# Kernel optimization log

Measured on AMD Instinct MI355X. Metric: run time of the kernel, lower is better.

Reference implementation:

```python
import jax, jax.numpy as jnp
import numpy as np

K = 1.0          # Lorentz curvature param: x_t^2 - |x_s|^2 = K
SQRT_K = 1.0
EPS = 1e-8
HEADS = 12

def add_time(s):
    t = jnp.sqrt(K + jnp.sum(s * s, axis=-1, keepdims=True))
    return jnp.concatenate([t, s], axis=-1)

def lorentz_ln(x, g, b):
    s = x[..., 1:]
    mu = jnp.mean(s, axis=-1, keepdims=True)
    var = jnp.var(s, axis=-1, keepdims=True)
    s = (s - mu) / jnp.sqrt(var + 1e-5) * g + b
    return add_time(s)

def lorentz_fc(x, W, heads=None, act=None):
    # linear on full Lorentz vector -> space part; time recomputed to stay on manifold
    s = x @ W.T
    if act is not None:
        s = act(s)
    if heads is not None:
        bsz, n, dt = s.shape
        s = s.reshape(bsz, n, heads, dt // heads).transpose(0, 2, 1, 3)  # (b,h,n,hd)
    return add_time(s)

def logmap0(x):
    t, s = x[..., :1], x[..., 1:]
    sn = jnp.sqrt(jnp.sum(s * s, axis=-1, keepdims=True))
    dist = SQRT_K * jnp.arccosh(jnp.maximum(t / SQRT_K, 1.0 + 1e-7))
    u = dist * s / jnp.maximum(sn, EPS)
    return jnp.concatenate([jnp.zeros_like(t), u], axis=-1)

def expmap0(u):
    us = u[..., 1:]
    n = jnp.sqrt(jnp.sum(us * us, axis=-1, keepdims=True))
    nc = jnp.maximum(n, EPS)
    t = SQRT_K * jnp.cosh(n / SQRT_K)
    s = SQRT_K * jnp.sinh(n / SQRT_K) * us / nc
    return jnp.concatenate([t, s], axis=-1)

def ste_clip(x, lo, hi):
    # straight-through estimator: clamp in fwd, identity grad
    return x + jax.lax.stop_gradient(jnp.clip(x, lo, hi) - x)

def ste_max_clamp(x, hi):
    return x + jax.lax.stop_gradient(jnp.minimum(x, hi) - x)

def mha_last_layer(x, Wq, Wk, Wv, Wo, alpha_raw, tau_raw, lambda_raw):
    q = lorentz_fc(x, Wq, heads=HEADS)   # (b,h,n,hd+1)
    k = lorentz_fc(x, Wk, heads=HEADS)
    v = lorentz_fc(x, Wv, heads=HEADS)
    q_t, q_s = q[..., :1], q[..., 1:]
    k_t, k_s = k[..., :1], k[..., 1:]
    # Lorentzian inner product -> hyperbolic pairwise distances
    inner_QK = -q_t @ jnp.swapaxes(k_t, -1, -2) + jnp.einsum('bhid,bhjd->bhij', q_s, k_s)
    raw_cosh = jnp.maximum(-inner_QK / K, 1.0)                # (b,h,n,n)
    is_self = raw_cosh < 1.0 + 1e-5
    safe_cosh = jnp.where(is_self, 2.0, raw_cosh)
    dist_QK = SQRT_K * jnp.arccosh(safe_cosh)
    cosh_OQ = jnp.maximum(q_t / SQRT_K, 1.0 + 1e-7)
    cosh_OK = jnp.maximum(k_t / SQRT_K, 1.0 + 1e-7)
    c_tilde = jnp.minimum(SQRT_K * jnp.arccosh(cosh_OQ), 40.0) / SQRT_K  # (b,h,n,1)
    sinh_QK = jnp.sinh(dist_QK / SQRT_K)
    sinh_OQ = jnp.sinh(c_tilde)
    numer = raw_cosh * cosh_OQ - jnp.swapaxes(cosh_OK, -1, -2)
    raw_Z = numer / (sinh_OQ * sinh_QK)
    Z_safe = jnp.where(is_self, 1.0, ste_clip(raw_Z, -1.0, 1.0))
    alpha = jax.nn.softplus(alpha_raw)
    B = alpha * c_tilde / (1.0 + alpha * c_tilde)
    lam = jax.nn.softplus(lambda_raw)
    d_L = ste_max_clamp(dist_QK, 40.0)   # float32 branch of STE_Dist_Clamp
    log_dist_penalty = -lam * jnp.log1p(d_L * d_L)
    m = 0.1
    entail = jax.nn.softplus(B + Z_safe - m) - jax.nn.softplus(jnp.asarray(-m, B.dtype))
    tau = jax.nn.softplus(tau_raw)
    score = jax.nn.softmax(log_dist_penalty - tau * entail, axis=-1)
    # expmap aggregation: tangent-space weighted mean
    v_tan = logmap0(v)
    agg = jnp.einsum('bhij,bhjd->bhid', score, v_tan)
    agg = agg / (jnp.sum(score, axis=-1, keepdims=True) + 1e-8)
    attn = expmap0(agg).transpose(0, 2, 1, 3)   # (b,n,h,hd+1)
    bsz, n, h, _ = attn.shape
    attn_s = attn[..., 1:].reshape(bsz, n, -1)
    attn_t = attn[..., :1].reshape(bsz, n, -1)
    t_new = jnp.sqrt(jnp.sum(attn_t ** 2, axis=-1, keepdims=True) - (h - 1) * K)
    return lorentz_fc(jnp.concatenate([t_new, attn_s], axis=-1), Wo)


def setup_inputs() -> dict:
    key = jax.random.key(0)
    ks = jax.random.split(key, 8)
    b, n, hidden, mlp_hidden = 4, 1024, 769, 3073
    d = hidden - 1
    xs = jax.random.normal(ks[0], (b, n, d), jnp.float32)
    x = add_time(xs)
    def w(k, o, i):
        return jax.random.normal(k, (o, i), jnp.float32) * (i ** -0.5)
    return {
        'x': x,
        'Wq': w(ks[1], d, hidden), 'Wk': w(ks[2], d, hidden), 'Wv': w(ks[3], d, hidden),
        'Wo': w(ks[4], d, hidden),
        'ln1_g': jnp.ones((d,), jnp.float32), 'ln1_b': jnp.zeros((d,), jnp.float32),
        'ln2_g': jnp.ones((d,), jnp.float32), 'ln2_b': jnp.zeros((d,), jnp.float32),
        'Wm1': w(ks[5], mlp_hidden - 1, hidden), 'Wm2': w(ks[6], d, mlp_hidden),
        'alpha_raw': jnp.zeros((1,), jnp.float32),
        'tau_raw': jnp.zeros((1,), jnp.float32),
        'lambda_raw': jnp.zeros((1,), jnp.float32),
    }


def reference(x, Wq, Wk, Wv, Wo, ln1_g, ln1_b, ln2_g, ln2_b, Wm1, Wm2, alpha_raw, tau_raw, lambda_raw):
    out = mha_last_layer(lorentz_ln(x, ln1_g, ln1_b), Wq, Wk, Wv, Wo, alpha_raw, tau_raw, lambda_raw)
    out = out[..., 1:] + x[..., 1:]                 # residual on space part (DropPath=identity in eval)
    h = lorentz_ln(add_time(out), ln2_g, ln2_b)
    h = lorentz_fc(h, Wm1, act=lambda z: jax.nn.gelu(z, approximate=False))
    h = lorentz_fc(h, Wm2)
    out = h[..., 1:] + out
    return add_time(out)
```

## Files before the change

kernel.cpp:

```cpp
#include <hip/hip_runtime.h>
#include <cstdint>
#include <cstddef>

typedef unsigned short u16;
typedef __attribute__((ext_vector_type(8))) __bf16 bf16x8;
typedef __attribute__((ext_vector_type(4))) float f32x4;
typedef __attribute__((ext_vector_type(4))) short s16x4;

#define SEQ 1024
#define MROWS 4096
#define DDIM 768
#define HID 769
#define KP1 832
#define MLPD 3072
#define KP2 3136
#define NHEADS 12
#define LN2F 0.69314718056f
#define LOG2EF 1.44269504089f

static __device__ __forceinline__ u16 f2bf(float f){
  union { float f; uint32_t u; } v; v.f = f;
  return (u16)((v.u + 0x7FFFu + ((v.u >> 16) & 1u)) >> 16);
}

static __device__ __forceinline__ f32x4 mfma16(bf16x8 a, bf16x8 b, f32x4 c){
  return __builtin_amdgcn_mfma_f32_16x16x32_bf16(a, b, c, 0, 0, 0);
}

static __device__ __forceinline__ f32x4 mfma16k(s16x4 a, s16x4 b, f32x4 c){
  return __builtin_amdgcn_mfma_f32_16x16x16bf16_1k(a, b, c, 0, 0, 0);
}

static __device__ __forceinline__ s16x4 pack4(uint32_t lo, uint32_t hi){
  union { uint2 u; s16x4 v; } cv; cv.u.x = lo; cv.u.y = hi; return cv.v;
}

static __device__ __forceinline__ void async_lds16(const u16* g, u16* l){
  u16* gm = const_cast<u16*>(g);
  __builtin_amdgcn_global_load_lds(
      (__attribute__((address_space(1))) void*)gm,
      (__attribute__((address_space(3))) void*)l, 16, 0, 0);
}

static __device__ __forceinline__ float blk_reduce(float v, float* red, int tid){
  #pragma unroll
  for (int off = 1; off < 64; off <<= 1) v += __shfl_xor(v, off, 64);
  __syncthreads();
  if ((tid & 63) == 0) red[tid >> 6] = v;
  __syncthreads();
  return red[0] + red[1] + red[2] + red[3];
}

static __device__ __forceinline__ float gelu_fast(float z){
  float z2 = z * z;
  float t = __builtin_fmaf(z2, 0.044715f, 1.f);
  float w = z * t * (-2.3022078f);
  float e2 = __builtin_amdgcn_exp2f(w);
  return z * __builtin_amdgcn_rcpf(1.f + e2);
}

static __device__ __forceinline__ void conv_seg(const float* W, u16* O, int idx, int K, int Kp){
  int n = idx / Kp, k = idx - n * Kp;
  O[idx] = (k < K) ? f2bf(W[(size_t)n * K + k]) : (u16)0;
}
__global__ __launch_bounds__(256) void conv_all(const float* __restrict__ Wq, const float* __restrict__ Wk,
    const float* __restrict__ Wv, const float* __restrict__ Wo,
    const float* __restrict__ Wm1, const float* __restrict__ Wm2, u16* __restrict__ dst){
  int b = blockIdx.x, tid = threadIdx.x;
  if (b < 2496){        conv_seg(Wq,  dst,            b*256+tid,         769, 832); }
  else if (b < 4992){   conv_seg(Wk,  dst + 638976,  (b-2496)*256+tid,   769, 832); }
  else if (b < 7488){   conv_seg(Wv,  dst + 1277952, (b-4992)*256+tid,   769, 832); }
  else if (b < 9984){   conv_seg(Wo,  dst + 1916928, (b-7488)*256+tid,   769, 832); }
  else if (b < 19968){  conv_seg(Wm1, dst + 2555904, (b-9984)*256+tid,   769, 832); }
  else {                conv_seg(Wm2, dst + 5111808, (b-19968)*256+tid, 3073, 3136); }
}

__global__ __launch_bounds__(256) void ln_kernel(const float* __restrict__ X, int xstr, int xoff,
    const float* __restrict__ g, const float* __restrict__ b, u16* __restrict__ O){
  __shared__ float red[4];
  int m = blockIdx.x, tid = threadIdx.x;
  const float* xr = X + (size_t)m * xstr + xoff;
  float s[3], y[3];
  float s1 = 0.f, s2 = 0.f;
  #pragma unroll
  for (int j = 0; j < 3; j++){ float v = xr[tid + j*256]; s[j] = v; s1 += v; s2 += v*v; }
  s1 = blk_reduce(s1, red, tid);
  s2 = blk_reduce(s2, red, tid);
  float mu = s1 * (1.f/768.f);
  float var = s2 * (1.f/768.f) - mu*mu;
  float rstd = rsqrtf(var + 1e-5f);
  float q = 0.f;
  #pragma unroll
  for (int j = 0; j < 3; j++){ int i = tid + j*256; y[j] = (s[j]-mu)*rstd*g[i] + b[i]; q += y[j]*y[j]; }
  q = blk_reduce(q, red, tid);
  u16* orow = O + (size_t)m * KP1;
  #pragma unroll
  for (int j = 0; j < 3; j++) orow[1 + tid + j*256] = f2bf(y[j]);
  if (tid == 0) orow[0] = f2bf(sqrtf(1.f + q));
  if (tid < 63) orow[769 + tid] = 0;
}

__global__ __launch_bounds__(256) void ln_sum_kernel(const float* __restrict__ P2,
    const float* __restrict__ x, const float* __restrict__ g, const float* __restrict__ b,
    float* __restrict__ out1, u16* __restrict__ O, float* __restrict__ rsq){
  __shared__ float red[4];
  int m = blockIdx.x, tid = threadIdx.x;
  if (tid == 0) rsq[m] = 0.f;
  float s[3], y[3];
  float s1 = 0.f, s2 = 0.f;
  #pragma unroll
  for (int j = 0; j < 3; j++){
    int col = tid + j*256;
    float v = x[(size_t)m * HID + 1 + col];
    #pragma unroll
    for (int z = 0; z < 2; z++) v += P2[(size_t)z*MROWS*DDIM + (size_t)m*DDIM + col];
    out1[(size_t)m*DDIM + col] = v;
    s[j] = v; s1 += v; s2 += v*v;
  }
  s1 = blk_reduce(s1, red, tid);
  s2 = blk_reduce(s2, red, tid);
  float mu = s1 * (1.f/768.f);
  float var = s2 * (1.f/768.f) - mu*mu;
  float rstd = rsqrtf(var + 1e-5f);
  float q = 0.f;
  #pragma unroll
  for (int j = 0; j < 3; j++){ int i = tid + j*256; y[j] = (s[j]-mu)*rstd*g[i] + b[i]; q += y[j]*y[j]; }
  q = blk_reduce(q, red, tid);
  u16* orow = O + (size_t)m * KP1;
  #pragma unroll
  for (int j = 0; j < 3; j++) orow[1 + tid + j*256] = f2bf(y[j]);
  if (tid == 0) orow[0] = f2bf(sqrtf(1.f + q));
  if (tid < 63) orow[769 + tid] = 0;
}

__global__ __launch_bounds__(256) void gemm64(
    const u16* __restrict__ A, const u16* __restrict__ B,
    float* __restrict__ C, u16* __restrict__ Og, float* __restrict__ rsq,
    int N, int Kp, int gelu)
{
  __shared__ u16 As[128*64];
  __shared__ u16 Bs[64*64];
  int tid = threadIdx.x;
  int wave = tid >> 6, lane = tid & 63;
  int lrow = lane & 15, lq = lane >> 4;
  int m0 = blockIdx.y * 128, n0 = blockIdx.x * 64;
  int wm = wave >> 1, wn = wave & 1;
  int chunks = Kp >> 6;
  int nz = gridDim.z, z = blockIdx.z;
  int base = chunks / nz, rem = chunks - base * nz;
  int begin = z * base + (z < rem ? z : rem);
  int count = base + (z < rem ? 1 : 0);
  f32x4 acc[4][2] = {};
  int srow = lane >> 3;
  int scol = (lane & 7) * 8;
  const u16* Abase = A + (size_t)m0 * Kp;
  const u16* Bbase = B + (size_t)n0 * Kp;
  for (int kc = begin; kc < begin + count; kc++){
    int k0 = kc * 64;
    __syncthreads();
    #pragma unroll
    for (int i = 0; i < 4; i++){
      int s = wave*4 + i;
      async_lds16(Abase + (size_t)(s*8 + srow) * Kp + k0 + scol, As + s*512);
    }
    #pragma unroll
    for (int i = 0; i < 2; i++){
      int s = wave*2 + i;
      async_lds16(Bbase + (size_t)(s*8 + srow) * Kp + k0 + scol, Bs + s*512);
    }
    __syncthreads();
    bf16x8 af[4][2], bfr[2][2];
    #pragma unroll
    for (int t = 0; t < 4; t++)
      #pragma unroll
      for (int kk = 0; kk < 2; kk++)
        af[t][kk] = *(const bf16x8*)(As + (wm*64 + t*16 + lrow)*64 + kk*32 + lq*8);
    #pragma unroll
    for (int t = 0; t < 2; t++)
      #pragma unroll
      for (int kk = 0; kk < 2; kk++)
        bfr[t][kk] = *(const bf16x8*)(Bs + (wn*32 + t*16 + lrow)*64 + kk*32 + lq*8);
    #pragma unroll
    for (int kk = 0; kk < 2; kk++)
      #pragma unroll
      for (int mt = 0; mt < 4; mt++)
        #pragma unroll
        for (int nt = 0; nt < 2; nt++)
          acc[mt][nt] = mfma16(af[mt][kk], bfr[nt][kk], acc[mt][nt]);
  }
  if (gelu == 0){
    C += (size_t)z * MROWS * N;
    #pragma unroll
    for (int mt = 0; mt < 4; mt++)
      #pragma unroll
      for (int nt = 0; nt < 2; nt++){
        int col = n0 + wn*32 + nt*16 + lrow;
        #pragma unroll
        for (int r = 0; r < 4; r++){
          int row = m0 + wm*64 + mt*16 + lq*4 + r;
          C[(size_t)row * N + col] = acc[mt][nt][r];
        }
      }
  } else {
    float ssq[4][4];
    #pragma unroll
    for (int mt = 0; mt < 4; mt++)
      #pragma unroll
      for (int r = 0; r < 4; r++) ssq[mt][r] = 0.f;
    #pragma unroll
    for (int mt = 0; mt < 4; mt++)
      #pragma unroll
      for (int nt = 0; nt < 2; nt++){
        int col = n0 + wn*32 + nt*16 + lrow;
        #pragma unroll
        for (int r = 0; r < 4; r++){
          int row = m0 + wm*64 + mt*16 + lq*4 + r;
          float e = gelu_fast(acc[mt][nt][r]);
          ssq[mt][r] += e*e;
          Og[(size_t)row * KP2 + 1 + col] = f2bf(e);
        }
      }
    #pragma unroll
    for (int mt = 0; mt < 4; mt++)
      #pragma unroll
      for (int r = 0; r < 4; r++){
        float v = ssq[mt][r];
        v += __shfl_xor(v, 1, 64);
        v += __shfl_xor(v, 2, 64);
        v += __shfl_xor(v, 4, 64);
        v += __shfl_xor(v, 8, 64);
        if (lrow == 0)
          atomicAdd(rsq + m0 + wm*64 + mt*16 + lq*4 + r, v);
      }
  }
}

__global__ __launch_bounds__(256) void timecol(const float* __restrict__ rsq, u16* __restrict__ O){
  int idx = blockIdx.x * 256 + threadIdx.x;
  int m = idx >> 6, j = idx & 63;
  if (j == 0) O[(size_t)m * KP2] = f2bf(sqrtf(1.f + rsq[m]));
  else        O[(size_t)m * KP2 + 3072 + j] = 0;
}

__global__ __launch_bounds__(256) void pack_qk(const float* __restrict__ raw,
    u16* __restrict__ Qp, u16* __restrict__ Kpk, float* __restrict__ qt, float* __restrict__ kt)
{
  int wave = threadIdx.x >> 6, lane = threadIdx.x & 63;
  int m = blockIdx.x * 4 + wave;
  int h = blockIdx.y;
  int which = blockIdx.z;
  const float* src = raw + (size_t)m * 2304 + which * 768 + h*64 + lane;
  float v = *src;
  float ss = v*v;
  #pragma unroll
  for (int off = 1; off < 64; off <<= 1) ss += __shfl_xor(ss, off, 64);
  int b = m >> 10, n = m & 1023, bh = b * NHEADS + h;
  u16* dst = (which ? Kpk : Qp) + ((size_t)bh * SEQ + n) * 64 + lane;
  *dst = f2bf(v);
  if (lane == 0) (which ? kt : qt)[bh * SEQ + n] = sqrtf(1.f + ss);
}

__global__ __launch_bounds__(256) void pack_v(const float* __restrict__ vraw, u16* __restrict__ Vf){
  __shared__ float part[256];
  __shared__ float scl[64];
  __shared__ float tile[64][65];
  int tid = threadIdx.x;
  int kb = blockIdx.x, bh = blockIdx.y;
  int b = bh / NHEADS, h = bh - b*NHEADS;
  int kl = tid >> 2;
  int d0 = (tid & 3) * 16;
  int m = b * SEQ + kb * 64 + kl;
  float v[16]; float ss = 0.f;
  const float* src = vraw + (size_t)m * 2304 + h*64 + d0;
  #pragma unroll
  for (int i = 0; i < 16; i++){ v[i] = src[i]; ss += v[i]*v[i]; }
  part[tid] = ss;
  __syncthreads();
  if ((tid & 3) == 0){
    float s2 = part[tid] + part[tid+1] + part[tid+2] + part[tid+3];
    float sn = sqrtf(s2);
    float tv = sqrtf(1.f + s2);
    float ctv = fmaxf(tv, 1.f + 1e-7f);
    float dist = __logf(ctv + sqrtf(fmaxf(ctv*ctv - 1.f, 0.f)));
    scl[kl] = dist / fmaxf(sn, 1e-8f);
  }
  __syncthreads();
  float sc = scl[kl];
  #pragma unroll
  for (int i = 0; i < 16; i++) tile[kl][d0 + i] = v[i] * sc;
  __syncthreads();
  #pragma unroll
  for (int i = 0; i < 2; i++){
    int idx = tid + i*256;
    int ctg_l = idx >> 7;
    int ntp = (idx >> 6) & 1;
    int ln  = idx & 63;
    int lr = ln & 15, lqq = ln >> 4;
    int k0 = ctg_l*16 + lqq*4;
    int dlo = ntp*32 + lr;
    u16 tmp[8];
    #pragma unroll
    for (int j = 0; j < 4; j++){
      tmp[j]     = f2bf(tile[k0+j][dlo]);
      tmp[4+j]   = f2bf(tile[k0+j][dlo+16]);
    }
    u16* dst = Vf + ((((size_t)bh*64 + kb*4 + ctg_l)*2 + ntp)*64 + ln)*8;
    *(uint4*)dst = *(const uint4*)tmp;
  }
}

__global__ __launch_bounds__(256) void attn_kernel(
    const u16* __restrict__ Q, const u16* __restrict__ K, const u16* __restrict__ Vf,
    const float* __restrict__ qt, const float* __restrict__ kt,
    float* __restrict__ pAgg, float* __restrict__ pDen,
    const float* __restrict__ a_raw, const float* __restrict__ t_raw, const float* __restrict__ l_raw)
{
  __shared__ float rv[4][64];
  int tid = threadIdx.x;
  int bh = blockIdx.y, ks = blockIdx.z;
  int qbase = blockIdx.x * 64;
  float alpha = __logf(1.f + __expf(a_raw[0]));
  float tau   = __logf(1.f + __expf(t_raw[0]));
  float lam   = __logf(1.f + __expf(l_raw[0]));
  if (tid < 64){
    float qtv = qt[bh * SEQ + qbase + tid];
    float cq = fmaxf(qtv, 1.f + 1e-7f);
    float A = cq + __builtin_amdgcn_sqrtf(fmaxf(cq*cq - 1.f, 0.f));
    float ct = fminf(__builtin_amdgcn_logf(A) * LN2F, 40.f);
    float e = __expf(ct);
    float sh = 0.5f * (e - __builtin_amdgcn_rcpf(e));
    float ac = alpha * ct;
    rv[0][tid] = qtv;
    rv[1][tid] = cq;
    rv[2][tid] = __builtin_amdgcn_rcpf(sh);
    rv[3][tid] = (ac * __builtin_amdgcn_rcpf(1.f + ac) - 0.1f) * LOG2EF;
  }
  __syncthreads();
  int wave = tid >> 6, lane = tid & 63;
  int lrow = lane & 15, lq = lane >> 4;
  int myrow = wave*16 + lrow;
  float qt_l = rv[0][myrow], cq_l = rv[1][myrow], rri_l = rv[2][myrow], Bw_l = rv[3][myrow];
  const float tbase = tau * 0.92967051f;
  const u16* Qb = Q + ((size_t)bh * SEQ + qbase + wave*16 + lrow) * 64 + lq*8;
  bf16x8 bq0 = *(const bf16x8*)Qb;
  bf16x8 bq1 = *(const bf16x8*)(Qb + 32);
  const u16* Kt = K + (size_t)bh * SEQ * 64 + (size_t)(ks*512 + lrow) * 64 + lq*8;
  const u16* Vp = Vf + (size_t)bh * 65536 + (size_t)(ks*32) * 1024 + lane*8;
  const float* ktp = kt + (size_t)bh * SEQ + ks*512 + lq*4;
  s16x4 ones;
  ones[0] = (short)0x3F80; ones[1] = (short)0x3F80; ones[2] = (short)0x3F80; ones[3] = (short)0x3F80;
  f32x4 o[4] = {};
  f32x4 dacc = {};
  for (int jt = 0; jt < 8; jt++){
    bf16x8 vv[8];
    #pragma unroll
    for (int ct = 0; ct < 4; ct++){
      vv[ct*2]   = *(const bf16x8*)(Vp + ct*1024);
      vv[ct*2+1] = *(const bf16x8*)(Vp + ct*1024 + 512);
    }
    float4 kv[4];
    #pragma unroll
    for (int ct = 0; ct < 4; ct++) kv[ct] = *(const float4*)(ktp + ct*16);
    f32x4 s[4];
    #pragma unroll
    for (int ct = 0; ct < 4; ct++){
      bf16x8 a0 = *(const bf16x8*)(Kt + ct*1024);
      bf16x8 a1 = *(const bf16x8*)(Kt + ct*1024 + 32);
      f32x4 z = {0.f, 0.f, 0.f, 0.f};
      z = mfma16(a0, bq0, z);
      z = mfma16(a1, bq1, z);
      s[ct] = z;
    }
    #pragma unroll
    for (int ct = 0; ct < 4; ct++){
      float4 kvv = kv[ct];
      uint32_t pu[4];
      #pragma unroll
      for (int r = 0; r < 4; r++){
        float ktv = (r == 0) ? kvv.x : (r == 1) ? kvv.y : (r == 2) ? kvv.z : kvv.w;
        float c = fmaxf(__builtin_fmaf(qt_l, ktv, -s[ct][r]), 1.f);
        bool self = c < 1.00001f;
        float ce = self ? 2.f : c;
        float cm1 = __builtin_fmaf(ce, ce, -1.f);
        float rs = __builtin_amdgcn_rsqf(cm1);
        float shq = cm1 * rs;
        float d = __builtin_amdgcn_logf(ce + shq) * LN2F;
        float L1 = __builtin_amdgcn_logf(__builtin_fmaf(d, d, 1.f));
        float Z = __builtin_fmaf(ce, cq_l, -ktv) * rri_l * rs;
        Z = fminf(fmaxf(Z, -1.f), 1.f);
        Z = self ? 1.f : Z;
        float w2 = __builtin_fmaf(Z, LOG2EF, Bw_l);
        float ew = __builtin_amdgcn_exp2f(w2);
        float L2 = __builtin_amdgcn_logf(ew + 1.f);
        float logit = __builtin_fmaf(-lam, L1, __builtin_fmaf(-tau, L2, tbase));
        float p = __builtin_amdgcn_exp2f(logit);
        pu[r] = __float_as_uint(p);
      }
      uint32_t lo = __builtin_amdgcn_perm(pu[1], pu[0], 0x07060302u);
      uint32_t hi = __builtin_amdgcn_perm(pu[3], pu[2], 0x07060302u);
      s16x4 pb = pack4(lo, hi);
      union { bf16x8 v8; s16x4 h[2]; } c0, c1;
      c0.v8 = vv[ct*2]; c1.v8 = vv[ct*2+1];
      o[0] = mfma16k(c0.h[0], pb, o[0]);
      o[1] = mfma16k(c0.h[1], pb, o[1]);
      o[2] = mfma16k(c1.h[0], pb, o[2]);
      o[3] = mfma16k(c1.h[1], pb, o[3]);
      dacc = mfma16k(ones, pb, dacc);
    }
    Kt += 4096; Vp += 4096; ktp += 64;
  }
  size_t rowb = (size_t)(ks*48 + bh) * SEQ + qbase + wave*16 + lrow;
  if (lq == 0) pDen[rowb] = dacc[0];
  #pragma unroll
  for (int nt = 0; nt < 4; nt++){
    float4 ov; ov.x = o[nt][0]; ov.y = o[nt][1]; ov.z = o[nt][2]; ov.w = o[nt][3];
    *(float4*)(pAgg + rowb * 64 + nt*16 + lq*4) = ov;
  }
}

__global__ __launch_bounds__(768) void expmap_pack(const float* __restrict__ pAgg,
    const float* __restrict__ pDen, u16* __restrict__ O){
  __shared__ float th2[NHEADS];
  int m = blockIdx.x, tid = threadIdx.x;
  int h = tid >> 6, lane = tid & 63;
  int b = m >> 10, n = m & 1023, bh = b*NHEADS + h;
  size_t i0 = ((size_t)bh * SEQ + n);
  size_t i1 = ((size_t)(48 + bh) * SEQ + n);
  float d = pDen[i0] + pDen[i1];
  float rden = __builtin_amdgcn_rcpf(d * (1.f + 1e-8f));
  float u = (pAgg[i0*64 + lane] + pAgg[i1*64 + lane]) * rden;
  float n2 = u*u;
  #pragma unroll
  for (int off = 1; off < 64; off <<= 1) n2 += __shfl_xor(n2, off, 64);
  float nn = sqrtf(n2);
  float e = __expf(nn);
  float ch = 0.5f * (e + 1.f/e);
  float sh = 0.5f * (e - 1.f/e);
  float sc = sh / fmaxf(nn, 1e-8f);
  u16* orow = O + (size_t)m * KP1;
  orow[1 + h*64 + lane] = f2bf(u * sc);
  if (lane == 0) th2[h] = ch*ch;
  __syncthreads();
  if (tid == 0){
    float ssum = 0.f;
    #pragma unroll
    for (int i = 0; i < NHEADS; i++) ssum += th2[i];
    orow[0] = f2bf(sqrtf(ssum - 11.f));
  }
  if (tid >= 1 && tid < 64) orow[768 + tid] = 0;
}

__global__ __launch_bounds__(256) void final_sum(const float* __restrict__ P4,
    const float* __restrict__ out1, float* __restrict__ out){
  __shared__ float red[4];
  int m = blockIdx.x, tid = threadIdx.x;
  float v[3]; float s2 = 0.f;
  #pragma unroll
  for (int j = 0; j < 3; j++){
    int col = tid + j*256;
    float t = out1[(size_t)m*DDIM + col];
    #pragma unroll
    for (int z = 0; z < 4; z++) t += P4[(size_t)z*MROWS*DDIM + (size_t)m*DDIM + col];
    v[j] = t; s2 += t*t;
  }
  s2 = blk_reduce(s2, red, tid);
  float* orow = out + (size_t)m * HID;
  if (tid == 0) orow[0] = sqrtf(1.f + s2);
  #pragma unroll
  for (int j = 0; j < 3; j++) orow[1 + tid + j*256] = v[j];
}

extern "C" void kernel_launch(void* const* d_in, const int* in_sizes, int n_in,
                              void* d_out, int out_size, void* d_ws, size_t ws_size,
                              hipStream_t stream)
{
  (void)in_sizes; (void)n_in; (void)out_size; (void)ws_size;
  const float* x   = (const float*)d_in[0];
  const float* Wq  = (const float*)d_in[1];
  const float* Wk  = (const float*)d_in[2];
  const float* Wv  = (const float*)d_in[3];
  const float* Wo  = (const float*)d_in[4];
  const float* g1p = (const float*)d_in[5];
  const float* b1p = (const float*)d_in[6];
  const float* g2p = (const float*)d_in[7];
  const float* b2p = (const float*)d_in[8];
  const float* Wm1 = (const float*)d_in[9];
  const float* Wm2 = (const float*)d_in[10];
  const float* ar  = (const float*)d_in[11];
  const float* tr  = (const float*)d_in[12];
  const float* lr  = (const float*)d_in[13];

  char* ws = (char*)d_ws;
  u16*   wqb  = (u16*)(ws + 0);
  u16*   wob  = (u16*)(ws + 3833856);
  u16*   wm1b = (u16*)(ws + 5111808);
  u16*   wm2b = (u16*)(ws + 10223616);
  u16*   xln  = (u16*)(ws + 15040512);
  float* qkv  = (float*)(ws + 21856256);
  u16*   qp   = (u16*)(ws + 59604992);
  u16*   kpk  = (u16*)(ws + 65896448);
  u16*   vf   = (u16*)(ws + 72187904);
  float* rsq  = (float*)(ws + 78479360);
  float* qtb  = (float*)(ws + 78495744);
  float* ktb  = (float*)(ws + 78692352);
  float* pAgg = (float*)(ws + 78888960);
  float* pDen = (float*)(ws + 104054784);
  u16*   woin = (u16*)(ws + 104448000);
  float* woP  = (float*)(ws + 21856256);
  u16*   ln2b = (u16*)(ws + 78888960);
  u16*   g1b  = (u16*)(ws + 21856256);
  float* out2P= (float*)(ws + 47546368);
  float* out1 = (float*)(ws + 97878016);

  conv_all<<<dim3(29376), 256, 0, stream>>>(Wq, Wk, Wv, Wo, Wm1, Wm2, wqb);
  ln_kernel<<<dim3(4096), 256, 0, stream>>>(x, 769, 1, g1p, b1p, xln);
  gemm64<<<dim3(36, 32, 1), 256, 0, stream>>>(xln, wqb, qkv, nullptr, nullptr, 2304, 832, 0);
  pack_qk<<<dim3(1024, 12, 2), 256, 0, stream>>>(qkv, qp, kpk, qtb, ktb);
  pack_v<<<dim3(16, 48), 256, 0, stream>>>(qkv + 1536, vf);
  attn_kernel<<<dim3(16, 48, 2), 256, 0, stream>>>(qp, kpk, vf, qtb, ktb, pAgg, pDen, ar, tr, lr);
  expmap_pack<<<dim3(4096), 768, 0, stream>>>(pAgg, pDen, woin);
  gemm64<<<dim3(12, 32, 2), 256, 0, stream>>>(woin, wob, woP, nullptr, nullptr, 768, 832, 0);
  ln_sum_kernel<<<dim3(4096), 256, 0, stream>>>(woP, x, g2p, b2p, out1, ln2b, rsq);
  gemm64<<<dim3(48, 32, 1), 256, 0, stream>>>(ln2b, wm1b, nullptr, g1b, rsq, 3072, 832, 1);
  timecol<<<dim3(1024), 256, 0, stream>>>(rsq, g1b);
  gemm64<<<dim3(12, 32, 4), 256, 0, stream>>>(g1b, wm2b, out2P, nullptr, nullptr, 768, 3136, 0);
  final_sum<<<dim3(4096), 256, 0, stream>>>(out2P, out1, (float*)d_out);
}
```

Measured before the change: 396.9 us.

## Pre-swizzle weights into MFMA fragment order and drop LDS staging in GEMMs

The weight conversion kernel now writes the bf16 weights in the exact per-lane MFMA fragment order, tiled by 64-column block and 64-wide K chunk. The GEMM then reads B fragments with coalesced direct global loads and A fragments straight from global memory, removing LDS staging and both barriers per K chunk. The cost is that A reuse across the two N-waves now goes through cache instead of shared memory. A-fragment loads are strided per row, so there is a risk of worse latency hiding and more memory traffic.

Result: slower. 516.4 us (+30.1%).

```diff
diff --git a/kernel.cpp b/kernel.cpp
--- a/kernel.cpp
+++ b/kernel.cpp
@@ -35,13 +35,6 @@
   union { uint2 u; s16x4 v; } cv; cv.u.x = lo; cv.u.y = hi; return cv.v;
 }
 
-static __device__ __forceinline__ void async_lds16(const u16* g, u16* l){
-  u16* gm = const_cast<u16*>(g);
-  __builtin_amdgcn_global_load_lds(
-      (__attribute__((address_space(1))) void*)gm,
-      (__attribute__((address_space(3))) void*)l, 16, 0, 0);
-}
-
 static __device__ __forceinline__ float blk_reduce(float v, float* red, int tid){
   #pragma unroll
   for (int off = 1; off < 64; off <<= 1) v += __shfl_xor(v, off, 64);
@@ -59,20 +52,39 @@
   return z * __builtin_amdgcn_rcpf(1.f + e2);
 }
 
-static __device__ __forceinline__ void conv_seg(const float* W, u16* O, int idx, int K, int Kp){
-  int n = idx / Kp, k = idx - n * Kp;
+static __device__ __forceinline__ void conv_frag(const float* W, u16* O, int idx,
+                                                 int K, int C_){
+  int j = idx & 7;
+  int lane = (idx >> 3) & 63;
+  int lq = lane >> 4, lrow = lane & 15;
+  int rest = idx >> 9;
+  int kk = rest & 1, nt = (rest >> 1) & 1, wn = (rest >> 2) & 1;
+  int kc = (rest >> 3) % C_, nblk = (rest >> 3) / C_;
+  int n = nblk*64 + wn*32 + nt*16 + lrow;
+  int k = kc*64 + kk*32 + lq*8 + j;
   O[idx] = (k < K) ? f2bf(W[(size_t)n * K + k]) : (u16)0;
 }
 __global__ __launch_bounds__(256) void conv_all(const float* __restrict__ Wq, const float* __restrict__ Wk,
     const float* __restrict__ Wv, const float* __restrict__ Wo,
     const float* __restrict__ Wm1, const float* __restrict__ Wm2, u16* __restrict__ dst){
   int b = blockIdx.x, tid = threadIdx.x;
-  if (b < 2496){        conv_seg(Wq,  dst,            b*256+tid,         769, 832); }
-  else if (b < 4992){   conv_seg(Wk,  dst + 638976,  (b-2496)*256+tid,   769, 832); }
-  else if (b < 7488){   conv_seg(Wv,  dst + 1277952, (b-4992)*256+tid,   769, 832); }
-  else if (b < 9984){   conv_seg(Wo,  dst + 1916928, (b-7488)*256+tid,   769, 832); }
-  else if (b < 19968){  conv_seg(Wm1, dst + 2555904, (b-9984)*256+tid,   769, 832); }
-  else {                conv_seg(Wm2, dst + 5111808, (b-19968)*256+tid, 3073, 3136); }
+  if (b < 7488){
+    int idx = b*256 + tid;
+    int j = idx & 7;
+    int lane = (idx >> 3) & 63;
+    int lq = lane >> 4, lrow = lane & 15;
+    int rest = idx >> 9;
+    int kk = rest & 1, nt = (rest >> 1) & 1, wn = (rest >> 2) & 1;
+    int kc = (rest >> 3) % 13, nblk = (rest >> 3) / 13;
+    int n = nblk*64 + wn*32 + nt*16 + lrow;
+    int k = kc*64 + kk*32 + lq*8 + j;
+    const float* W = (n < 768) ? Wq : (n < 1536 ? Wk : Wv);
+    int nn = (n < 768) ? n : (n < 1536 ? n - 768 : n - 1536);
+    dst[idx] = (k < 769) ? f2bf(W[(size_t)nn * 769 + k]) : (u16)0;
+  }
+  else if (b < 9984){  conv_frag(Wo,  dst + 1916928, (b-7488)*256+tid,  769, 13); }
+  else if (b < 19968){ conv_frag(Wm1, dst + 2555904, (b-9984)*256+tid,  769, 13); }
+  else {               conv_frag(Wm2, dst + 5111808, (b-19968)*256+tid, 3073, 49); }
 }
 
 __global__ __launch_bounds__(256) void ln_kernel(const float* __restrict__ X, int xstr, int xoff,
@@ -133,17 +145,16 @@
   if (tid < 63) orow[769 + tid] = 0;
 }
 
-__global__ __launch_bounds__(256) void gemm64(
-    const u16* __restrict__ A, const u16* __restrict__ B,
+__global__ __launch_bounds__(256) void gemm_frag(
+    const u16* __restrict__ A, const u16* __restrict__ Bf,
     float* __restrict__ C, u16* __restrict__ Og, float* __restrict__ rsq,
     int N, int Kp, int gelu)
 {
-  __shared__ u16 As[128*64];
-  __shared__ u16 Bs[64*64];
   int tid = threadIdx.x;
   int wave = tid >> 6, lane = tid & 63;
   int lrow = lane & 15, lq = lane >> 4;
-  int m0 = blockIdx.y * 128, n0 = blockIdx.x * 64;
+  int m0 = blockIdx.y * 128;
+  int nblk = blockIdx.x;
   int wm = wave >> 1, wn = wave & 1;
   int chunks = Kp >> 6;
   int nz = gridDim.z, z = blockIdx.z;
@@ -151,35 +162,20 @@
   int begin = z * base + (z < rem ? z : rem);
   int count = base + (z < rem ? 1 : 0);
   f32x4 acc[4][2] = {};
-  int srow = lane >> 3;
-  int scol = (lane & 7) * 8;
-  const u16* Abase = A + (size_t)m0 * Kp;
-  const u16* Bbase = B + (size_t)n0 * Kp;
-  for (int kc = begin; kc < begin + count; kc++){
-    int k0 = kc * 64;
-    __syncthreads();
-    #pragma unroll
-    for (int i = 0; i < 4; i++){
-      int s = wave*4 + i;
-      async_lds16(Abase + (size_t)(s*8 + srow) * Kp + k0 + scol, As + s*512);
-    }
-    #pragma unroll
-    for (int i = 0; i < 2; i++){
-      int s = wave*2 + i;
-      async_lds16(Bbase + (size_t)(s*8 + srow) * Kp + k0 + scol, Bs + s*512);
-    }
-    __syncthreads();
+  const u16* Ab = A + (size_t)(m0 + wm*64 + lrow) * Kp + begin*64 + lq*8;
+  const u16* Bb = Bf + (((size_t)nblk * chunks + begin)*2 + wn) * 2048 + lane*8;
+  for (int kc = 0; kc < count; kc++){
     bf16x8 af[4][2], bfr[2][2];
     #pragma unroll
-    for (int t = 0; t < 4; t++)
+    for (int mt = 0; mt < 4; mt++)
       #pragma unroll
       for (int kk = 0; kk < 2; kk++)
-        af[t][kk] = *(const bf16x8*)(As + (wm*64 + t*16 + lrow)*64 + kk*32 + lq*8);
-    #pragma unroll
-    for (int t = 0; t < 2; t++)
+        af[mt][kk] = *(const bf16x8*)(Ab + (size_t)mt*16*Kp + kk*32);
+    #pragma unroll
+    for (int nt = 0; nt < 2; nt++)
       #pragma unroll
       for (int kk = 0; kk < 2; kk++)
-        bfr[t][kk] = *(const bf16x8*)(Bs + (wn*32 + t*16 + lrow)*64 + kk*32 + lq*8);
+        bfr[nt][kk] = *(const bf16x8*)(Bb + nt*1024 + kk*512);
     #pragma unroll
     for (int kk = 0; kk < 2; kk++)
       #pragma unroll
@@ -187,6 +183,7 @@
         #pragma unroll
         for (int nt = 0; nt < 2; nt++)
           acc[mt][nt] = mfma16(af[mt][kk], bfr[nt][kk], acc[mt][nt]);
+    Ab += 64; Bb += 4096;
   }
   if (gelu == 0){
     C += (size_t)z * MROWS * N;
@@ -194,7 +191,7 @@
     for (int mt = 0; mt < 4; mt++)
       #pragma unroll
       for (int nt = 0; nt < 2; nt++){
-        int col = n0 + wn*32 + nt*16 + lrow;
+        int col = nblk*64 + wn*32 + nt*16 + lrow;
         #pragma unroll
         for (int r = 0; r < 4; r++){
           int row = m0 + wm*64 + mt*16 + lq*4 + r;
@@ -211,7 +208,7 @@
     for (int mt = 0; mt < 4; mt++)
       #pragma unroll
       for (int nt = 0; nt < 2; nt++){
-        int col = n0 + wn*32 + nt*16 + lrow;
+        int col = nblk*64 + wn*32 + nt*16 + lrow;
         #pragma unroll
         for (int r = 0; r < 4; r++){
           int row = m0 + wm*64 + mt*16 + lq*4 + r;
@@ -514,15 +511,15 @@
 
   conv_all<<<dim3(29376), 256, 0, stream>>>(Wq, Wk, Wv, Wo, Wm1, Wm2, wqb);
   ln_kernel<<<dim3(4096), 256, 0, stream>>>(x, 769, 1, g1p, b1p, xln);
-  gemm64<<<dim3(36, 32, 1), 256, 0, stream>>>(xln, wqb, qkv, nullptr, nullptr, 2304, 832, 0);
+  gemm_frag<<<dim3(36, 32, 1), 256, 0, stream>>>(xln, wqb, qkv, nullptr, nullptr, 2304, 832, 0);
   pack_qk<<<dim3(1024, 12, 2), 256, 0, stream>>>(qkv, qp, kpk, qtb, ktb);
   pack_v<<<dim3(16, 48), 256, 0, stream>>>(qkv + 1536, vf);
   attn_kernel<<<dim3(16, 48, 2), 256, 0, stream>>>(qp, kpk, vf, qtb, ktb, pAgg, pDen, ar, tr, lr);
   expmap_pack<<<dim3(4096), 768, 0, stream>>>(pAgg, pDen, woin);
-  gemm64<<<dim3(12, 32, 2), 256, 0, stream>>>(woin, wob, woP, nullptr, nullptr, 768, 832, 0);
+  gemm_frag<<<dim3(12, 32, 2), 256, 0, stream>>>(woin, wob, woP, nullptr, nullptr, 768, 832, 0);
   ln_sum_kernel<<<dim3(4096), 256, 0, stream>>>(woP, x, g2p, b2p, out1, ln2b, rsq);
-  gemm64<<<dim3(48, 32, 1), 256, 0, stream>>>(ln2b, wm1b, nullptr, g1b, rsq, 3072, 832, 1);
+  gemm_frag<<<dim3(48, 32, 1), 256, 0, stream>>>(ln2b, wm1b, nullptr, g1b, rsq, 3072, 832, 1);
   timecol<<<dim3(1024), 256, 0, stream>>>(rsq, g1b);
-  gemm64<<<dim3(12, 32, 4), 256, 0, stream>>>(g1b, wm2b, out2P, nullptr, nullptr, 768, 3136, 0);
+  gemm_frag<<<dim3(12, 32, 4), 256, 0, stream>>>(g1b, wm2b, out2P, nullptr, nullptr, 768, 3136, 0);
   final_sum<<<dim3(4096), 256, 0, stream>>>(out2P, out1, (float*)d_out);
 }
```
